# Performance work log

Measured on AMD Instinct MI355X. Metric: run time of the kernel, lower is better.

## Reference

```python
import jax, jax.numpy as jnp
import numpy as np

B, L, H, E = 32, 2048, 1024, 512


def setup_inputs() -> dict:
    key = jax.random.key(0)
    ks = jax.random.split(key, 11)
    s = 0.02
    return {
        "h": jax.random.normal(ks[0], (B, H), jnp.float32),
        "x": jax.random.normal(ks[1], (B, E), jnp.float32),
        "contexts": jax.random.normal(ks[2], (B, L, H), jnp.float32),
        "W_enc": jax.random.normal(ks[3], (H, H), jnp.float32) * s,
        "b_enc": jnp.zeros((H,), jnp.float32),
        "W_dec": jax.random.normal(ks[4], (H, H), jnp.float32) * s,
        "b_dec": jnp.zeros((H,), jnp.float32),
        "W_v": jax.random.normal(ks[5], (H,), jnp.float32) * s,  # linear_v weight, out_dim=1
        "b_v": jnp.zeros((), jnp.float32),
        "W_r": jax.random.normal(ks[6], (2 * H + E, 2 * H), jnp.float32) * s,
        "b_r": jnp.zeros((2 * H,), jnp.float32),
    }


def reference(h, x, contexts, W_enc, b_enc, W_dec, b_dec, W_v, b_v, W_r, b_r):
    # additive (Bahdanau) score: v^T tanh(W_e @ ctx + W_d @ h)
    gamma_enc = jnp.einsum("blh,hk->blk", contexts, W_enc) + b_enc       # [B,L,H]
    gamma_dec = (h @ W_dec + b_dec)[:, None, :]                           # [B,1,H]
    scores = jnp.tanh(gamma_enc + gamma_dec) @ W_v + b_v                  # [B,L]
    weights = jax.nn.softmax(scores, axis=1)                              # [B,L]
    c_t = jnp.einsum("bl,blh->bh", weights, contexts)                     # [B,H]
    r_t = jnp.concatenate([c_t, h, x], axis=1) @ W_r + b_r                # [B,2H]
    # maxout: view(-1, H, 2).max(2)
    output = jnp.max(r_t.reshape(-1, H, 2), axis=2)                       # [B,H]
    return output, weights
```

## Files before the change

kernel.cpp:

```cpp
#include <hip/hip_runtime.h>
#include <hip/hip_bf16.h>

typedef unsigned short u16;
typedef __attribute__((ext_vector_type(8))) short bf16x8;
typedef __attribute__((ext_vector_type(4))) float f32x4;

#define B_   32
#define L_   2048
#define H_   1024
#define E_   512
#define KCAT 2560
#define NR   2048

__device__ __align__(256) u16   g_WencT[H_*H_];
__device__ __align__(256) u16   g_ctx16[(size_t)B_*L_*H_];
__device__ __align__(256) float g_gdec[B_*H_];
__device__ __align__(256) float g_scores[B_*L_];
__device__ __align__(256) float g_cat[B_*KCAT];
__device__ __align__(256) float g_pct[32][B_*H_];
__device__ __align__(256) float g_part[40][B_*NR];

__device__ __forceinline__ u16 f2b(float f) {
  unsigned x = __float_as_uint(f);
  return (u16)((x + 0x7fffu + ((x >> 16) & 1u)) >> 16);
}
__device__ __forceinline__ float b2f(u16 u) {
  return __uint_as_float(((unsigned)u) << 16);
}

__device__ __forceinline__ void gll16(const void* g, void* l) {
  __builtin_amdgcn_global_load_lds(
      (const __attribute__((address_space(1))) void*)g,
      (__attribute__((address_space(3))) void*)l, 16, 0, 0);
}

__device__ __forceinline__ float tanh_fast(float x) {
  float e = __expf(2.0f * x);
  return 1.0f - 2.0f / (e + 1.0f);
}

__global__ __launch_bounds__(256) void k_transpose(const float* __restrict__ W) {
  __shared__ float t[64 * 65];
  const int n0 = blockIdx.x * 64, k0 = blockIdx.y * 64;
  const int c = threadIdx.x & 63, q = threadIdx.x >> 6;
  #pragma unroll
  for (int rr = 0; rr < 16; rr++) {
    int r = rr * 4 + q;
    t[c * 65 + r] = W[(size_t)(k0 + r) * H_ + n0 + c];
  }
  __syncthreads();
  #pragma unroll
  for (int nn = 0; nn < 16; nn++) {
    int nl = nn * 4 + q;
    g_WencT[(size_t)(n0 + nl) * H_ + k0 + c] = f2b(t[nl * 65 + c]);
  }
}

__global__ __launch_bounds__(256) void k_cvt(const float* __restrict__ ctx) {
  const size_t gid = (size_t)blockIdx.x * 256 + threadIdx.x;
  #pragma unroll
  for (int it = 0; it < 8; it++) {
    const size_t c = gid + (size_t)it * 1048576;
    const float4 a = *(const float4*)(ctx + c * 8);
    const float4 b = *(const float4*)(ctx + c * 8 + 4);
    bf16x8 o;
    o[0] = (short)f2b(a.x); o[1] = (short)f2b(a.y);
    o[2] = (short)f2b(a.z); o[3] = (short)f2b(a.w);
    o[4] = (short)f2b(b.x); o[5] = (short)f2b(b.y);
    o[6] = (short)f2b(b.z); o[7] = (short)f2b(b.w);
    *(bf16x8*)&g_ctx16[c * 8] = o;
  }
}

__global__ __launch_bounds__(256) void k_init(const float* __restrict__ h,
                                              const float* __restrict__ x,
                                              const float* __restrict__ b_enc,
                                              const float* __restrict__ b_dec,
                                              const float* __restrict__ b_v) {
  int id = blockIdx.x * 256 + threadIdx.x;
  if (id < 32768) { g_gdec[id] = b_dec[id & 1023] + b_enc[id & 1023]; return; }
  id -= 32768;
  if (id < 65536) { g_scores[id] = b_v[0]; return; }
  id -= 65536;
  {
    int b = id / KCAT, c = id - b * KCAT;
    float v = 0.0f;
    if (c >= 1024 && c < 2048) v = h[b * H_ + (c - 1024)];
    else if (c >= 2048)        v = x[b * E_ + (c - 2048)];
    g_cat[id] = v;
  }
}

__global__ __launch_bounds__(256) void k_gdec(const float* __restrict__ h,
                                              const float* __restrict__ Wd) {
  const int b = blockIdx.y;
  const int hc = blockIdx.x & 3, kc = blockIdx.x >> 2;
  const int col = hc * 256 + threadIdx.x;
  const float* hb = h + b * H_ + kc * 256;
  const float* wp = Wd + (size_t)(kc * 256) * H_ + col;
  float acc = 0.0f;
  #pragma unroll 8
  for (int k = 0; k < 256; k++) acc = fmaf(hb[k], wp[(size_t)k * H_], acc);
  atomicAdd(&g_gdec[b * H_ + col], acc);
}

#define BK 64
__global__ __launch_bounds__(512, 2) void k_scores(const float* __restrict__ Wv) {
  __shared__ u16 Ab[2][256 * BK];
  __shared__ u16 Bb[2][256 * BK];
  __shared__ float ssum[256];
  const int tid = threadIdx.x;

  const int orig = blockIdx.x;
  const int wg = (orig & 7) * 128 + (orig >> 3);
  const int mtile = wg >> 2;
  const int ntile = wg & 3;
  const int b  = mtile >> 3;
  const int l0 = (mtile & 7) * 256;

  const char* Asrc = (const char*)(g_ctx16 + ((size_t)(b * L_ + l0)) * H_);
  const char* Bsrc = (const char*)(g_WencT + (size_t)(ntile * 256) * H_);

  size_t soff[4];
  #pragma unroll
  for (int q = 0; q < 4; q++) {
    const int sid = q * 512 + tid;
    const int row = sid >> 3, slot = sid & 7;
    soff[q] = (size_t)row * 2048 + (size_t)((slot ^ (row & 7)) << 4);
  }

  const int lane = tid & 63, wid = tid >> 6;
  const int wm = wid >> 2, wn = wid & 3;
  const int r16 = lane & 15, g = lane >> 4;
  const int base_a = (wm * 128 + r16) * BK;
  const int base_b = (wn * 64 + r16) * BK;

  if (tid < 256) ssum[tid] = 0.0f;

  f32x4 acc[8][4];
  #pragma unroll
  for (int i = 0; i < 8; i++)
    #pragma unroll
    for (int j = 0; j < 4; j++) acc[i][j] = (f32x4)0.0f;

  auto stage = [&](int buf, int ks) {
    const size_t kb = (size_t)ks * 128;
    #pragma unroll
    for (int q = 0; q < 4; q++)
      gll16(Asrc + soff[q] + kb, (char*)&Ab[buf][0] + q * 8192 + tid * 16);
    #pragma unroll
    for (int q = 0; q < 4; q++)
      gll16(Bsrc + soff[q] + kb, (char*)&Bb[buf][0] + q * 8192 + tid * 16);
  };

  stage(0, 0);
  __syncthreads();

  for (int ks = 0; ks < 16; ks++) {
    const int cur = ks & 1;
    if (ks < 15) stage(cur ^ 1, ks + 1);
    #pragma unroll
    for (int kk = 0; kk < 2; kk++) {
      const int po = (((kk * 4 + g) ^ (r16 & 7)) << 3);
      bf16x8 bf0 = *(const bf16x8*)&Bb[cur][base_b + 0 * 1024 + po];
      bf16x8 bf1 = *(const bf16x8*)&Bb[cur][base_b + 1 * 1024 + po];
      bf16x8 bf2 = *(const bf16x8*)&Bb[cur][base_b + 2 * 1024 + po];
      bf16x8 bf3 = *(const bf16x8*)&Bb[cur][base_b + 3 * 1024 + po];
      #pragma unroll
      for (int mt = 0; mt < 8; mt++) {
        bf16x8 am = *(const bf16x8*)&Ab[cur][base_a + mt * 1024 + po];
        acc[mt][0] = __builtin_amdgcn_mfma_f32_16x16x32_bf16(am, bf0, acc[mt][0], 0, 0, 0);
        acc[mt][1] = __builtin_amdgcn_mfma_f32_16x16x32_bf16(am, bf1, acc[mt][1], 0, 0, 0);
        acc[mt][2] = __builtin_amdgcn_mfma_f32_16x16x32_bf16(am, bf2, acc[mt][2], 0, 0, 0);
        acc[mt][3] = __builtin_amdgcn_mfma_f32_16x16x32_bf16(am, bf3, acc[mt][3], 0, 0, 0);
      }
    }
    __syncthreads();
  }

  const int colb = ntile * 256 + wn * 64;
  float wv[4], gd[4];
  #pragma unroll
  for (int q = 0; q < 4; q++) {
    const int col = colb + q * 16 + r16;
    wv[q] = Wv[col];
    gd[q] = g_gdec[b * H_ + col];
  }
  #pragma unroll
  for (int mt = 0; mt < 8; mt++) {
    #pragma unroll
    for (int r = 0; r < 4; r++) {
      float p = 0.0f;
      #pragma unroll
      for (int q = 0; q < 4; q++)
        p += tanh_fast(acc[mt][q][r] + gd[q]) * wv[q];
      p += __shfl_xor(p, 1);
      p += __shfl_xor(p, 2);
      p += __shfl_xor(p, 4);
      p += __shfl_xor(p, 8);
      if (r16 == 0) atomicAdd(&ssum[wm * 128 + mt * 16 + g * 4 + r], p);
    }
  }
  __syncthreads();
  if (tid < 256) atomicAdd(&g_scores[b * L_ + l0 + tid], ssum[tid]);
}

__global__ __launch_bounds__(256) void k_softmax(float* __restrict__ wout) {
  const int b = blockIdx.x, tid = threadIdx.x;
  __shared__ float red[4];
  float v[8]; float m = -1e30f;
  #pragma unroll
  for (int i = 0; i < 8; i++) {
    v[i] = g_scores[b * L_ + i * 256 + tid];
    m = fmaxf(m, v[i]);
  }
  #pragma unroll
  for (int s = 1; s < 64; s <<= 1) m = fmaxf(m, __shfl_xor(m, s));
  if ((tid & 63) == 0) red[tid >> 6] = m;
  __syncthreads();
  m = fmaxf(fmaxf(red[0], red[1]), fmaxf(red[2], red[3]));
  __syncthreads();
  float s = 0.0f;
  #pragma unroll
  for (int i = 0; i < 8; i++) { v[i] = __expf(v[i] - m); s += v[i]; }
  #pragma unroll
  for (int t = 1; t < 64; t <<= 1) s += __shfl_xor(s, t);
  if ((tid & 63) == 0) red[tid >> 6] = s;
  __syncthreads();
  const float inv = 1.0f / (red[0] + red[1] + red[2] + red[3]);
  #pragma unroll
  for (int i = 0; i < 8; i++) wout[b * L_ + i * 256 + tid] = v[i] * inv;
}

__global__ __launch_bounds__(256) void k_ct(const float* __restrict__ wout) {
  const int lc = blockIdx.x, b = blockIdx.y;
  const int cg = threadIdx.x & 127, rh = threadIdx.x >> 7;
  __shared__ float wl[128];
  if (threadIdx.x < 128) wl[threadIdx.x] = wout[b * L_ + lc * 128 + threadIdx.x];
  __syncthreads();
  const u16* cp = g_ctx16 + ((size_t)(b * L_ + lc * 128 + rh * 64)) * H_ + cg * 8;
  float a[8] = {0.f, 0.f, 0.f, 0.f, 0.f, 0.f, 0.f, 0.f};
  #pragma unroll 8
  for (int i = 0; i < 64; i++) {
    const bf16x8 v = *(const bf16x8*)(cp + (size_t)i * H_);
    const float w = wl[rh * 64 + i];
    #pragma unroll
    for (int j = 0; j < 8; j++) a[j] = fmaf(b2f((u16)v[j]), w, a[j]);
  }
  #pragma unroll
  for (int j = 0; j < 8; j++)
    g_pct[lc * 2 + rh][b * H_ + cg * 8 + j] = a[j];
}

__global__ __launch_bounds__(256) void k_ctred() {
  const int id = blockIdx.x * 256 + threadIdx.x;
  float s = 0.0f;
  #pragma unroll 8
  for (int lc = 0; lc < 32; lc++) s += g_pct[lc][id];
  g_cat[(id >> 10) * KCAT + (id & 1023)] = s;
}

__global__ __launch_bounds__(256) void k_r1(const float* __restrict__ Wr) {
  const int nc = blockIdx.x, kc = blockIdx.y, tid = threadIdx.x;
  __shared__ float cl[32][64];
  #pragma unroll
  for (int i = 0; i < 8; i++) {
    int flat = i * 256 + tid;
    cl[flat >> 6][flat & 63] = g_cat[(flat >> 6) * KCAT + kc * 64 + (flat & 63)];
  }
  __syncthreads();
  float acc[32];
  #pragma unroll
  for (int b2 = 0; b2 < 32; b2++) acc[b2] = 0.0f;
  const float* wp = Wr + (size_t)(kc * 64) * NR + nc * 256 + tid;
  #pragma unroll 4
  for (int k4 = 0; k4 < 16; k4++) {
    float w0 = wp[(size_t)(k4 * 4 + 0) * NR], w1 = wp[(size_t)(k4 * 4 + 1) * NR],
          w2 = wp[(size_t)(k4 * 4 + 2) * NR], w3 = wp[(size_t)(k4 * 4 + 3) * NR];
    #pragma unroll
    for (int b2 = 0; b2 < 32; b2++) {
      const float4 c4 = *(const float4*)&cl[b2][k4 * 4];
      acc[b2] = fmaf(c4.x, w0, acc[b2]);
      acc[b2] = fmaf(c4.y, w1, acc[b2]);
      acc[b2] = fmaf(c4.z, w2, acc[b2]);
      acc[b2] = fmaf(c4.w, w3, acc[b2]);
    }
  }
  float* pp = &g_part[kc][nc * 256 + tid];
  #pragma unroll
  for (int b2 = 0; b2 < 32; b2++) pp[b2 * NR] = acc[b2];
}

__global__ __launch_bounds__(256) void k_maxout(const float* __restrict__ b_r,
                                                float* __restrict__ out) {
  const int id = blockIdx.x * 256 + threadIdx.x;
  const int j = id & 1023;
  float r0 = b_r[2 * j], r1 = b_r[2 * j + 1];
  #pragma unroll 8
  for (int kc = 0; kc < 40; kc++) {
    const float2 v = *(const float2*)&g_part[kc][2 * id];
    r0 += v.x; r1 += v.y;
  }
  out[id] = fmaxf(r0, r1);
}

extern "C" void kernel_launch(void* const* d_in, const int* in_sizes, int n_in,
                              void* d_out, int out_size, void* d_ws, size_t ws_size,
                              hipStream_t stream) {
  (void)in_sizes; (void)n_in; (void)d_ws; (void)ws_size; (void)out_size;
  const float* h     = (const float*)d_in[0];
  const float* x     = (const float*)d_in[1];
  const float* ctx   = (const float*)d_in[2];
  const float* W_enc = (const float*)d_in[3];
  const float* b_enc = (const float*)d_in[4];
  const float* W_dec = (const float*)d_in[5];
  const float* b_dec = (const float*)d_in[6];
  const float* W_v   = (const float*)d_in[7];
  const float* b_v   = (const float*)d_in[8];
  const float* W_r   = (const float*)d_in[9];
  const float* b_r   = (const float*)d_in[10];
  float* out  = (float*)d_out;
  float* wout = out + 32768;

  k_transpose<<<dim3(16, 16), 256, 0, stream>>>(W_enc);
  k_cvt<<<4096, 256, 0, stream>>>(ctx);
  k_init<<<704, 256, 0, stream>>>(h, x, b_enc, b_dec, b_v);
  k_gdec<<<dim3(16, 32), 256, 0, stream>>>(h, W_dec);
  k_scores<<<1024, 512, 0, stream>>>(W_v);
  k_softmax<<<32, 256, 0, stream>>>(wout);
  k_ct<<<dim3(16, 32), 256, 0, stream>>>(wout);
  k_ctred<<<128, 256, 0, stream>>>();
  k_r1<<<dim3(8, 40), 256, 0, stream>>>(W_r);
  k_maxout<<<128, 256, 0, stream>>>(b_r, out);
}
```

Baseline: 669.3 us.

## Split scores GEMM K-stages into halves with vmcnt-gated single-barrier pipeline

Each 64-wide K tile of the scores GEMM is now staged as two 32-wide halves in separate LDS buffers, giving a finer-grained software pipeline. The full __syncthreads per stage is replaced with an s_waitcnt vmcnt plus a single s_barrier, so several async loads stay in flight while waves compute. All A/B fragments are loaded into registers before the MFMA burst, which is wrapped in s_setprio to favour matrix issue. The LDS swizzle is simplified to a 4-slot XOR. The last iterations issue redundant wrap-around loads, and the hand-counted vmcnt must match the actual number of outstanding loads.

```diff
diff --git a/kernel.cpp b/kernel.cpp
--- a/kernel.cpp
+++ b/kernel.cpp
@@ -106,8 +106,8 @@
 
 #define BK 64
 __global__ __launch_bounds__(512, 2) void k_scores(const float* __restrict__ Wv) {
-  __shared__ u16 Ab[2][256 * BK];
-  __shared__ u16 Bb[2][256 * BK];
+  __shared__ u16 Ab[2][2][256 * 32];
+  __shared__ u16 Bb[2][2][256 * 32];
   __shared__ float ssum[256];
   const int tid = threadIdx.x;
 
@@ -121,19 +121,20 @@
   const char* Asrc = (const char*)(g_ctx16 + ((size_t)(b * L_ + l0)) * H_);
   const char* Bsrc = (const char*)(g_WencT + (size_t)(ntile * 256) * H_);
 
-  size_t soff[4];
-  #pragma unroll
-  for (int q = 0; q < 4; q++) {
+  size_t soff[2];
+  #pragma unroll
+  for (int q = 0; q < 2; q++) {
     const int sid = q * 512 + tid;
-    const int row = sid >> 3, slot = sid & 7;
-    soff[q] = (size_t)row * 2048 + (size_t)((slot ^ (row & 7)) << 4);
+    const int row = sid >> 2, ps = sid & 3;
+    soff[q] = (size_t)row * 2048 + (size_t)((ps ^ (row & 3)) << 4);
   }
 
   const int lane = tid & 63, wid = tid >> 6;
   const int wm = wid >> 2, wn = wid & 3;
   const int r16 = lane & 15, g = lane >> 4;
-  const int base_a = (wm * 128 + r16) * BK;
-  const int base_b = (wn * 64 + r16) * BK;
+  const int swz = ((g ^ (r16 & 3)) << 3);
+  const int aoff = (wm * 128 + r16) * 32 + swz;
+  const int boff = (wn * 64 + r16) * 32 + swz;
 
   if (tid < 256) ssum[tid] = 0.0f;
 
@@ -143,39 +144,43 @@
     #pragma unroll
     for (int j = 0; j < 4; j++) acc[i][j] = (f32x4)0.0f;
 
-  auto stage = [&](int buf, int ks) {
-    const size_t kb = (size_t)ks * 128;
-    #pragma unroll
-    for (int q = 0; q < 4; q++)
-      gll16(Asrc + soff[q] + kb, (char*)&Ab[buf][0] + q * 8192 + tid * 16);
-    #pragma unroll
-    for (int q = 0; q < 4; q++)
-      gll16(Bsrc + soff[q] + kb, (char*)&Bb[buf][0] + q * 8192 + tid * 16);
+  auto stage = [&](int buf, int half, int ks) {
+    const size_t kb = (size_t)ks * 128 + (size_t)half * 64;
+    #pragma unroll
+    for (int q = 0; q < 2; q++) {
+      gll16(Asrc + soff[q] + kb, (char*)&Ab[buf][half][0] + q * 8192 + tid * 16);
+      gll16(Bsrc + soff[q] + kb, (char*)&Bb[buf][half][0] + q * 8192 + tid * 16);
+    }
   };
 
-  stage(0, 0);
-  __syncthreads();
-
-  for (int ks = 0; ks < 16; ks++) {
-    const int cur = ks & 1;
-    if (ks < 15) stage(cur ^ 1, ks + 1);
-    #pragma unroll
-    for (int kk = 0; kk < 2; kk++) {
-      const int po = (((kk * 4 + g) ^ (r16 & 7)) << 3);
-      bf16x8 bf0 = *(const bf16x8*)&Bb[cur][base_b + 0 * 1024 + po];
-      bf16x8 bf1 = *(const bf16x8*)&Bb[cur][base_b + 1 * 1024 + po];
-      bf16x8 bf2 = *(const bf16x8*)&Bb[cur][base_b + 2 * 1024 + po];
-      bf16x8 bf3 = *(const bf16x8*)&Bb[cur][base_b + 3 * 1024 + po];
-      #pragma unroll
-      for (int mt = 0; mt < 8; mt++) {
-        bf16x8 am = *(const bf16x8*)&Ab[cur][base_a + mt * 1024 + po];
-        acc[mt][0] = __builtin_amdgcn_mfma_f32_16x16x32_bf16(am, bf0, acc[mt][0], 0, 0, 0);
-        acc[mt][1] = __builtin_amdgcn_mfma_f32_16x16x32_bf16(am, bf1, acc[mt][1], 0, 0, 0);
-        acc[mt][2] = __builtin_amdgcn_mfma_f32_16x16x32_bf16(am, bf2, acc[mt][2], 0, 0, 0);
-        acc[mt][3] = __builtin_amdgcn_mfma_f32_16x16x32_bf16(am, bf3, acc[mt][3], 0, 0, 0);
-      }
+  stage(0, 0, 0);
+  stage(0, 1, 0);
+
+  #pragma unroll 2
+  for (int p = 0; p < 32; p++) {
+    const int t = p >> 1, kk = p & 1;
+    const int cur = t & 1;
+    stage(cur ^ 1, kk, (t + 1) & 15);
+    asm volatile("s_waitcnt vmcnt(8)" ::: "memory");
+    __builtin_amdgcn_s_barrier();
+
+    const u16* Ah = &Ab[cur][kk][0];
+    const u16* Bh = &Bb[cur][kk][0];
+    bf16x8 bfv[4], af[8];
+    #pragma unroll
+    for (int nt = 0; nt < 4; nt++) bfv[nt] = *(const bf16x8*)&Bh[boff + nt * 512];
+    #pragma unroll
+    for (int mt = 0; mt < 8; mt++) af[mt] = *(const bf16x8*)&Ah[aoff + mt * 512];
+
+    __builtin_amdgcn_s_setprio(1);
+    #pragma unroll
+    for (int mt = 0; mt < 8; mt++) {
+      acc[mt][0] = __builtin_amdgcn_mfma_f32_16x16x32_bf16(af[mt], bfv[0], acc[mt][0], 0, 0, 0);
+      acc[mt][1] = __builtin_amdgcn_mfma_f32_16x16x32_bf16(af[mt], bfv[1], acc[mt][1], 0, 0, 0);
+      acc[mt][2] = __builtin_amdgcn_mfma_f32_16x16x32_bf16(af[mt], bfv[2], acc[mt][2], 0, 0, 0);
+      acc[mt][3] = __builtin_amdgcn_mfma_f32_16x16x32_bf16(af[mt], bfv[3], acc[mt][3], 0, 0, 0);
     }
-    __syncthreads();
+    __builtin_amdgcn_s_setprio(0);
   }
 
   const int colb = ntile * 256 + wn * 64;
```

Measured after the change: 657.8 us. Within noise of the previous version (-1.7%).
